# Kernel optimization log

Hardware: AMD Instinct MI355X
Metric: run time of the kernel (lower is better)

## Reference

```python
import jax, jax.numpy as jnp
import numpy as np

B, Lq, C, NH, NP, DFF = 8, 10000, 256, 8, 4, 1024
H_IMG, W_IMG = 100, 100
HD = C // NH


def _layer_norm(x, g, b, eps=1e-5):
    m = jnp.mean(x, -1, keepdims=True)
    v = jnp.mean((x - m) ** 2, -1, keepdims=True)
    return (x - m) / jnp.sqrt(v + eps) * g + b


def _bilinear_sample(value, loc, Hs, Ws):
    # value: [B, Lin, NH, HD]; loc: [B, Lq, NH, NP, 2] normalized to [0,1]
    vt = jnp.transpose(value, (0, 2, 1, 3))  # [B, NH, Lin, HD]
    # move to [B, NH, Lq, NP] layout once; grid_sample(align_corners=False) pixel coords
    x = jnp.transpose(loc[..., 0], (0, 2, 1, 3)) * Ws - 0.5
    y = jnp.transpose(loc[..., 1], (0, 2, 1, 3)) * Hs - 0.5
    x0 = jnp.floor(x); y0 = jnp.floor(y)
    lx = x - x0; ly = y - y0

    def corner(xi, yi, w):
        valid = (xi >= 0) & (xi < Ws) & (yi >= 0) & (yi < Hs)
        xc = jnp.clip(xi, 0, Ws - 1).astype(jnp.int32)
        yc = jnp.clip(yi, 0, Hs - 1).astype(jnp.int32)
        idx = (yc * Ws + xc).reshape(B, NH, Lq * NP, 1)
        v = jnp.take_along_axis(vt, idx, axis=2).reshape(B, NH, Lq, NP, HD)
        return v * (w * valid)[..., None]

    acc = corner(x0, y0, (1 - lx) * (1 - ly))
    acc = acc + corner(x0 + 1, y0, lx * (1 - ly))
    acc = acc + corner(x0, y0 + 1, (1 - lx) * ly)
    acc = acc + corner(x0 + 1, y0 + 1, lx * ly)
    return acc  # [B, NH, Lq, NP, HD]


def setup_inputs() -> dict:
    key = jax.random.key(0)
    ks = jax.random.split(key, 12)
    s = 0.02
    return {
        "query": jax.random.normal(ks[0], (B, Lq, C), jnp.float32),
        "src": jax.random.normal(ks[1], (B, H_IMG * W_IMG, C), jnp.float32),
        "reference_points": jax.random.uniform(ks[2], (B, Lq, 1, 2), jnp.float32),
        "spatial_shapes": jnp.array([[H_IMG, W_IMG]], dtype=jnp.int64),
        "level_start_index": jnp.array([0], dtype=jnp.int64),
        "W_off": jax.random.normal(ks[3], (C, NH * NP * 2), jnp.float32) * s,
        "b_off": jnp.zeros((NH * NP * 2,), jnp.float32),
        "W_aw": jax.random.normal(ks[4], (C, NH * NP), jnp.float32) * s,
        "b_aw": jnp.zeros((NH * NP,), jnp.float32),
        "W_val": jax.random.normal(ks[5], (C, C), jnp.float32) * s,
        "b_val": jnp.zeros((C,), jnp.float32),
        "W_out": jax.random.normal(ks[6], (C, C), jnp.float32) * s,
        "b_out": jnp.zeros((C,), jnp.float32),
        "g1": jnp.ones((C,), jnp.float32),
        "be1": jnp.zeros((C,), jnp.float32),
        "W1": jax.random.normal(ks[7], (C, DFF), jnp.float32) * s,
        "b1": jnp.zeros((DFF,), jnp.float32),
        "W2": jax.random.normal(ks[8], (DFF, C), jnp.float32) * s,
        "b2": jnp.zeros((C,), jnp.float32),
        "g2": jnp.ones((C,), jnp.float32),
        "be2": jnp.zeros((C,), jnp.float32),
    }


def reference(query, src, reference_points, spatial_shapes, level_start_index,
              W_off, b_off, W_aw, b_aw, W_val, b_val, W_out, b_out,
              g1, be1, W1, b1, W2, b2, g2, be2):
    Hs = spatial_shapes[0, 0]
    Ws = spatial_shapes[0, 1]
    # MSDeformAttn (n_levels = 1)
    value = (src @ W_val + b_val).reshape(B, -1, NH, HD)
    off = (query @ W_off + b_off).reshape(B, Lq, NH, NP, 2)
    aw = jax.nn.softmax((query @ W_aw + b_aw).reshape(B, Lq, NH, NP), axis=-1)
    normalizer = jnp.stack([Ws, Hs]).astype(query.dtype)  # (W, H)
    loc = reference_points[:, :, None] + off / normalizer  # [B,Lq,NH,NP,2]
    sampled = _bilinear_sample(value, loc, Hs, Ws)  # [B,NH,Lq,NP,HD]
    attn = jnp.einsum('bhqpd,bqhp->bqhd', sampled, aw).reshape(B, Lq, C)
    attn = attn @ W_out + b_out
    # residual + LN + FFN + LN
    q = _layer_norm(query + attn, g1, be1)
    ffn = jax.nn.relu(q @ W1 + b1) @ W2 + b2
    return _layer_norm(q + ffn, g2, be2)
```

## Files before the change

kernel.cpp:

```cpp
#include <hip/hip_runtime.h>
#include <hip/hip_bf16.h>

typedef __hip_bfloat16 bf16;
typedef unsigned short u16;
typedef short short8 __attribute__((ext_vector_type(8)));
typedef float f32x4 __attribute__((ext_vector_type(4)));

static constexpr int B_   = 8;
static constexpr int Lq_  = 10000;
static constexpr int C_   = 256;
static constexpr int NH_  = 8;
static constexpr int NP_  = 4;
static constexpr int HIMG = 100;
static constexpr int WIMG = 100;
static constexpr int LIN  = 10000;

__device__ __forceinline__ u16 f2bf(float x) {
    union { bf16 b; u16 u; } cv; cv.b = __float2bfloat16(x); return cv.u;
}
__device__ __forceinline__ float bf2f(u16 u) {
    return __uint_as_float((unsigned)u << 16);
}

__device__ __forceinline__ void gl_lds16(const void* g, void* l) {
    __builtin_amdgcn_global_load_lds(
        (const __attribute__((address_space(1))) void*)g,
        (__attribute__((address_space(3))) void*)l, 16, 0, 0);
}
__device__ __forceinline__ void drain_barrier() {
    asm volatile("s_waitcnt vmcnt(0) lgkmcnt(0)" ::: "memory");
    __builtin_amdgcn_s_barrier();
}


template <bool AF32, bool LN>
__global__ __launch_bounds__(512, 2) void gemm256(
    const void* __restrict__ Av, const u16* __restrict__ Bg,
    const float* __restrict__ bias, const float* __restrict__ resid,
    const float* __restrict__ gw, const float* __restrict__ bw,
    u16* __restrict__ Co, int K)
{
    __shared__ __align__(16) u16 At[2][128 * 64];
    __shared__ __align__(16) u16 Bt[2][256 * 64];
    __shared__ float red[2][128][4];

    const int tid  = threadIdx.x;
    const int lane = tid & 63;
    const int w    = tid >> 6;
    const int wm   = w >> 2, wn = w & 3;
    const int m0   = blockIdx.x * 128;

    f32x4 acc[4][4];
#pragma unroll
    for (int i = 0; i < 4; ++i)
#pragma unroll
        for (int j = 0; j < 4; ++j) acc[i][j] = f32x4{0.f, 0.f, 0.f, 0.f};

    auto stageA = [&](int t) {
        const int kt = t << 6;
        if constexpr (AF32) {
            const int row = tid >> 2;
            const int k0  = (tid & 3) << 4;
            const float* s = (const float*)Av + (size_t)(m0 + row) * K + kt + k0;
            float4 v0 = *(const float4*)(s + 0);
            float4 v1 = *(const float4*)(s + 4);
            float4 v2 = *(const float4*)(s + 8);
            float4 v3 = *(const float4*)(s + 12);
            union { short8 s8; u16 u[8]; } ga, gb;
            ga.u[0]=f2bf(v0.x); ga.u[1]=f2bf(v0.y); ga.u[2]=f2bf(v0.z); ga.u[3]=f2bf(v0.w);
            ga.u[4]=f2bf(v1.x); ga.u[5]=f2bf(v1.y); ga.u[6]=f2bf(v1.z); ga.u[7]=f2bf(v1.w);
            gb.u[0]=f2bf(v2.x); gb.u[1]=f2bf(v2.y); gb.u[2]=f2bf(v2.z); gb.u[3]=f2bf(v2.w);
            gb.u[4]=f2bf(v3.x); gb.u[5]=f2bf(v3.y); gb.u[6]=f2bf(v3.z); gb.u[7]=f2bf(v3.w);
            u16* d = &At[t & 1][row * 64];
            *(short8*)&d[(k0)     ^ ((row & 7) << 3)] = ga.s8;
            *(short8*)&d[(k0 + 8) ^ ((row & 7) << 3)] = gb.s8;
        } else {
#pragma unroll
            for (int i = 0; i < 2; ++i) {
                const int rb  = w * 16 + i * 8;
                const int row = rb + (lane >> 3);
                const int gs  = (lane & 7) ^ (row & 7);
                gl_lds16((const u16*)Av + (size_t)(m0 + row) * K + kt + gs * 8,
                         &At[t & 1][rb * 64]);
            }
        }
    };
    auto stageB = [&](int t) {
        const int kt = t << 6;
#pragma unroll
        for (int i = 0; i < 4; ++i) {
            const int rb  = w * 32 + i * 8;
            const int row = rb + (lane >> 3);
            gl_lds16(Bg + (size_t)row * K + kt + (lane & 7) * 8,
                     &Bt[t & 1][rb * 64]);
        }
    };
    auto compute = [&](int t) {
        const u16* a = At[t & 1];
        const u16* b = Bt[t & 1];
#pragma unroll
        for (int ks = 0; ks < 2; ++ks) {
            const int ko = ks * 32 + ((lane >> 4) << 3);
            short8 bfr[4];
#pragma unroll
            for (int n = 0; n < 4; ++n) {
                const int nr = wn * 64 + n * 16 + (lane & 15);
                bfr[n] = *(const short8*)&b[nr * 64 + (ko ^ ((nr & 7) << 3))];
            }
#pragma unroll
            for (int m = 0; m < 4; ++m) {
                const int ar = wm * 64 + m * 16 + (lane & 15);
                const short8 af = *(const short8*)&a[ar * 64 + (ko ^ ((ar & 7) << 3))];
#pragma unroll
                for (int n = 0; n < 4; ++n)
                    acc[m][n] = __builtin_amdgcn_mfma_f32_16x16x32_bf16(
                        af, bfr[n], acc[m][n], 0, 0, 0);
            }
        }
    };

    stageA(0); stageB(0);
    drain_barrier();
    const int nt = K >> 6;
    for (int t = 0; t < nt; ++t) {
        if (t + 1 < nt) { stageA(t + 1); stageB(t + 1); }
        compute(t);
        drain_barrier();
    }

    float bcol[4], gcol[4], becol[4];
#pragma unroll
    for (int n = 0; n < 4; ++n) {
        const int col = wn * 64 + n * 16 + (lane & 15);
        bcol[n] = bias[col];
        if (LN) { gcol[n] = gw[col]; becol[n] = bw[col]; }
    }

    if constexpr (!LN) {
#pragma unroll
        for (int m = 0; m < 4; ++m)
#pragma unroll
            for (int r = 0; r < 4; ++r) {
                const int lr = wm * 64 + m * 16 + (lane >> 4) * 4 + r;
#pragma unroll
                for (int n = 0; n < 4; ++n) {
                    const int col = wn * 64 + n * 16 + (lane & 15);
                    Co[(size_t)(m0 + lr) * 256 + col] = f2bf(acc[m][n][r] + bcol[n]);
                }
            }
    } else {
        float s[4][4], s2[4][4];
#pragma unroll
        for (int m = 0; m < 4; ++m)
#pragma unroll
            for (int r = 0; r < 4; ++r) {
                const int lr = wm * 64 + m * 16 + (lane >> 4) * 4 + r;
                float ps = 0.f, ps2 = 0.f;
#pragma unroll
                for (int n = 0; n < 4; ++n) {
                    const int col = wn * 64 + n * 16 + (lane & 15);
                    float v = acc[m][n][r] + bcol[n]
                            + resid[(size_t)(m0 + lr) * 256 + col];
                    acc[m][n][r] = v;
                    ps += v; ps2 += v * v;
                }
#pragma unroll
                for (int o = 1; o < 16; o <<= 1) {
                    ps  += __shfl_xor(ps,  o);
                    ps2 += __shfl_xor(ps2, o);
                }
                s[m][r] = ps; s2[m][r] = ps2;
            }
        if ((lane & 15) == 0) {
#pragma unroll
            for (int m = 0; m < 4; ++m)
#pragma unroll
                for (int r = 0; r < 4; ++r) {
                    const int lr = wm * 64 + m * 16 + (lane >> 4) * 4 + r;
                    red[0][lr][wn] = s[m][r];
                    red[1][lr][wn] = s2[m][r];
                }
        }
        __syncthreads();
        if (tid < 128) {
            const float ss  = red[0][tid][0] + red[0][tid][1] + red[0][tid][2] + red[0][tid][3];
            const float ss2 = red[1][tid][0] + red[1][tid][1] + red[1][tid][2] + red[1][tid][3];
            const float mean = ss * (1.f / 256.f);
            const float var  = fmaxf(ss2 * (1.f / 256.f) - mean * mean, 0.f);
            red[0][tid][0] = mean;
            red[1][tid][0] = rsqrtf(var + 1e-5f);
        }
        __syncthreads();
#pragma unroll
        for (int m = 0; m < 4; ++m)
#pragma unroll
            for (int r = 0; r < 4; ++r) {
                const int lr = wm * 64 + m * 16 + (lane >> 4) * 4 + r;
                const float mean = red[0][lr][0];
                const float rstd = red[1][lr][0];
#pragma unroll
                for (int n = 0; n < 4; ++n) {
                    const int col = wn * 64 + n * 16 + (lane & 15);
                    const float o = (acc[m][n][r] - mean) * rstd * gcol[n] + becol[n];
                    Co[(size_t)(m0 + lr) * 256 + (col ^ ((lr & 7) << 3))] = f2bf(o);
                }
            }
    }
}

__global__ __launch_bounds__(512, 2) void ffn_fused(
    const u16* __restrict__ q1b, const u16* __restrict__ W1s,
    const u16* __restrict__ W2s, const float* __restrict__ b1,
    const float* __restrict__ b2, const float* __restrict__ g2,
    const float* __restrict__ be2, float* __restrict__ out)
{
    __shared__ __align__(16) u16 As[128 * 256];
    __shared__ __align__(16) u16 Hs[128 * 128];
    __shared__ __align__(16) u16 B1t[2][128 * 32];
    __shared__ __align__(16) u16 B2t[2][256 * 32];
    __shared__ float red[2][128][4];

    const int tid  = threadIdx.x;
    const int lane = tid & 63;
    const int w    = tid >> 6;
    const int wm   = w >> 2, wn = w & 3;
    const int m0   = blockIdx.x * 128;

    f32x4 acc2[4][4];
#pragma unroll
    for (int i = 0; i < 4; ++i)
#pragma unroll
        for (int j = 0; j < 4; ++j) acc2[i][j] = f32x4{0.f, 0.f, 0.f, 0.f};

    auto stageB1 = [&](int c, int t) {
        const int rb  = w * 16;
        const int row = rb + (lane >> 2);
        gl_lds16(W1s + (size_t)(c * 128 + row) * 256 + t * 32 + (lane & 3) * 8,
                 &B1t[t & 1][rb * 32]);
    };
    auto stageB2 = [&](int c, int t) {
#pragma unroll
        for (int i = 0; i < 2; ++i) {
            const int rb  = i * 128 + w * 16;
            const int row = rb + (lane >> 2);
            gl_lds16(W2s + (size_t)row * 1024 + c * 128 + t * 32 + (lane & 3) * 8,
                     &B2t[t & 1][rb * 32]);
        }
    };

#pragma unroll
    for (int i = 0; i < 8; ++i) {
        const int rb = w * 16 + i * 2;
        gl_lds16(q1b + (size_t)(m0 + rb + (lane >> 5)) * 256 + (lane & 31) * 8,
                 &As[rb * 256]);
    }
    stageB1(0, 0);
    drain_barrier();

    for (int c = 0; c < 8; ++c) {
        f32x4 acc1[4][2];
#pragma unroll
        for (int i = 0; i < 4; ++i)
#pragma unroll
            for (int j = 0; j < 2; ++j) acc1[i][j] = f32x4{0.f, 0.f, 0.f, 0.f};

        for (int t = 0; t < 8; ++t) {
            if (t < 7) stageB1(c, t + 1);
            else       stageB2(c, 0);
            const u16* b = B1t[t & 1];
            const int ko = (lane >> 4) << 3;
            short8 bfr[2];
#pragma unroll
            for (int n = 0; n < 2; ++n) {
                const int nr = wn * 32 + n * 16 + (lane & 15);
                bfr[n] = *(const short8*)&b[nr * 32 + (ko ^ ((nr & 3) << 3))];
            }
#pragma unroll
            for (int m = 0; m < 4; ++m) {
                const int ar = wm * 64 + m * 16 + (lane & 15);
                const short8 af = *(const short8*)
                    &As[ar * 256 + ((t * 32 + ko) ^ ((ar & 7) << 3))];
#pragma unroll
                for (int n = 0; n < 2; ++n)
                    acc1[m][n] = __builtin_amdgcn_mfma_f32_16x16x32_bf16(
                        af, bfr[n], acc1[m][n], 0, 0, 0);
            }
            drain_barrier();
        }

#pragma unroll
        for (int n = 0; n < 2; ++n) {
            const int col = wn * 32 + n * 16 + (lane & 15);
            const float bb = b1[c * 128 + col];
#pragma unroll
            for (int m = 0; m < 4; ++m)
#pragma unroll
                for (int r = 0; r < 4; ++r) {
                    const int row = wm * 64 + m * 16 + (lane >> 4) * 4 + r;
                    const float hv = fmaxf(acc1[m][n][r] + bb, 0.f);
                    Hs[row * 128 + (col ^ ((row & 7) << 3))] = f2bf(hv);
                }
        }
        asm volatile("s_waitcnt lgkmcnt(0)" ::: "memory");
        __builtin_amdgcn_s_barrier();

        for (int t = 0; t < 4; ++t) {
            if (t < 3)      stageB2(c, t + 1);
            else if (c < 7) stageB1(c + 1, 0);
            const u16* b = B2t[t & 1];
            const int ko = (lane >> 4) << 3;
            short8 bfr[4];
#pragma unroll
            for (int n = 0; n < 4; ++n) {
                const int nr = wn * 64 + n * 16 + (lane & 15);
                bfr[n] = *(const short8*)&b[nr * 32 + (ko ^ ((nr & 3) << 3))];
            }
#pragma unroll
            for (int m = 0; m < 4; ++m) {
                const int hr = wm * 64 + m * 16 + (lane & 15);
                const short8 af = *(const short8*)
                    &Hs[hr * 128 + ((t * 32 + ko) ^ ((hr & 7) << 3))];
#pragma unroll
                for (int n = 0; n < 4; ++n)
                    acc2[m][n] = __builtin_amdgcn_mfma_f32_16x16x32_bf16(
                        af, bfr[n], acc2[m][n], 0, 0, 0);
            }
            drain_barrier();
        }
    }

    float bcol[4], gcol[4], becol[4];
#pragma unroll
    for (int n = 0; n < 4; ++n) {
        const int col = wn * 64 + n * 16 + (lane & 15);
        bcol[n] = b2[col]; gcol[n] = g2[col]; becol[n] = be2[col];
    }
    float s[4][4], s2[4][4];
#pragma unroll
    for (int m = 0; m < 4; ++m)
#pragma unroll
        for (int r = 0; r < 4; ++r) {
            const int lr = wm * 64 + m * 16 + (lane >> 4) * 4 + r;
            float ps = 0.f, ps2 = 0.f;
#pragma unroll
            for (int n = 0; n < 4; ++n) {
                const int col = wn * 64 + n * 16 + (lane & 15);
                const float q = bf2f(As[lr * 256 + (col ^ ((lr & 7) << 3))]);
                const float v = acc2[m][n][r] + bcol[n] + q;
                acc2[m][n][r] = v;
                ps += v; ps2 += v * v;
            }
#pragma unroll
            for (int o = 1; o < 16; o <<= 1) {
                ps  += __shfl_xor(ps,  o);
                ps2 += __shfl_xor(ps2, o);
            }
            s[m][r] = ps; s2[m][r] = ps2;
        }
    if ((lane & 15) == 0) {
#pragma unroll
        for (int m = 0; m < 4; ++m)
#pragma unroll
            for (int r = 0; r < 4; ++r) {
                const int lr = wm * 64 + m * 16 + (lane >> 4) * 4 + r;
                red[0][lr][wn] = s[m][r];
                red[1][lr][wn] = s2[m][r];
            }
    }
    __syncthreads();
    if (tid < 128) {
        const float ss  = red[0][tid][0] + red[0][tid][1] + red[0][tid][2] + red[0][tid][3];
        const float ss2 = red[1][tid][0] + red[1][tid][1] + red[1][tid][2] + red[1][tid][3];
        const float mean = ss * (1.f / 256.f);
        const float var  = fmaxf(ss2 * (1.f / 256.f) - mean * mean, 0.f);
        red[0][tid][0] = mean;
        red[1][tid][0] = rsqrtf(var + 1e-5f);
    }
    __syncthreads();
#pragma unroll
    for (int m = 0; m < 4; ++m)
#pragma unroll
        for (int r = 0; r < 4; ++r) {
            const int lr = wm * 64 + m * 16 + (lane >> 4) * 4 + r;
            const float mean = red[0][lr][0];
            const float rstd = red[1][lr][0];
#pragma unroll
            for (int n = 0; n < 4; ++n) {
                const int col = wn * 64 + n * 16 + (lane & 15);
                out[(size_t)(m0 + lr) * 256 + col] =
                    (acc2[m][n][r] - mean) * rstd * gcol[n] + becol[n];
            }
        }
}

__global__ __launch_bounds__(256) void gemm_oaw(
    const float* __restrict__ Av, const u16* __restrict__ Bt,
    const float* __restrict__ bias, float* __restrict__ C,
    int M, int K, int Nreal, int ldc)
{
    __shared__ __align__(16) u16 Asl[2][128 * 32];
    __shared__ __align__(16) u16 Bsl[2][128 * 32];

    const int tid  = threadIdx.x;
    const int lane = tid & 63;
    const int w    = tid >> 6;
    const int wr   = (w >> 1) * 64;
    const int wc   = (w & 1) * 64;
    const int m0   = blockIdx.y * 128;
    const int n0   = blockIdx.x * 128;

    const int srow = lane >> 2;
    const int scol = (lane & 3) << 3;
    const u16* bG = Bt + (size_t)(n0 + w * 32 + srow) * K + scol;
    const size_t rstep16 = (size_t)16 * K;

    const int ar  = lane >> 3;
    const int ac  = (lane & 7) << 2;
    const float* aGf = Av + (size_t)(m0 + w * 32 + ar) * K + ac;

    const int aRoff = (wr + (lane & 15)) * 32 + (lane >> 4) * 8;
    const int bRoff = (wc + (lane & 15)) * 32 + (lane >> 4) * 8;

    f32x4 acc[4][4];
#pragma unroll
    for (int i = 0; i < 4; ++i)
#pragma unroll
        for (int j = 0; j < 4; ++j) acc[i][j] = f32x4{0.f, 0.f, 0.f, 0.f};

    float4 a4[4];
    const int nt = K >> 5;

#pragma unroll
    for (int rep = 0; rep < 4; ++rep)
        a4[rep] = *(const float4*)(aGf + (size_t)(rep * 8) * K);
#pragma unroll
    for (int rep = 0; rep < 4; ++rep) {
        ushort4 v{f2bf(a4[rep].x), f2bf(a4[rep].y), f2bf(a4[rep].z), f2bf(a4[rep].w)};
        *(ushort4*)&Asl[0][(w * 32 + rep * 8 + ar) * 32 + ac] = v;
    }
    gl_lds16(bG, &Bsl[0][(w * 32) * 32]);
    gl_lds16(bG + rstep16, &Bsl[0][(w * 32 + 16) * 32]);
    drain_barrier();

    for (int t = 0; t < nt; ++t) {
        const int cur = t & 1, nxt = cur ^ 1;
        const int k0n = (t + 1) << 5;
        const bool has_next = (t + 1 < nt);
        if (has_next) {
#pragma unroll
            for (int rep = 0; rep < 4; ++rep)
                a4[rep] = *(const float4*)(aGf + k0n + (size_t)(rep * 8) * K);
            gl_lds16(bG + k0n, &Bsl[nxt][(w * 32) * 32]);
            gl_lds16(bG + k0n + rstep16, &Bsl[nxt][(w * 32 + 16) * 32]);
        }
        short8 af[4], bfr[4];
#pragma unroll
        for (int m = 0; m < 4; ++m) af[m]  = *(const short8*)&Asl[cur][aRoff + m * 16 * 32];
#pragma unroll
        for (int n = 0; n < 4; ++n) bfr[n] = *(const short8*)&Bsl[cur][bRoff + n * 16 * 32];
#pragma unroll
        for (int m = 0; m < 4; ++m)
#pragma unroll
            for (int n = 0; n < 4; ++n)
                acc[m][n] = __builtin_amdgcn_mfma_f32_16x16x32_bf16(
                    af[m], bfr[n], acc[m][n], 0, 0, 0);
        if (has_next) {
#pragma unroll
            for (int rep = 0; rep < 4; ++rep) {
                ushort4 v{f2bf(a4[rep].x), f2bf(a4[rep].y), f2bf(a4[rep].z), f2bf(a4[rep].w)};
                *(ushort4*)&Asl[nxt][(w * 32 + rep * 8 + ar) * 32 + ac] = v;
            }
        }
        drain_barrier();
    }

#pragma unroll
    for (int n = 0; n < 4; ++n) {
        const int gc = n0 + wc + n * 16 + (lane & 15);
        if (gc >= Nreal) continue;
        const float bv = bias[gc];
        const int gr0 = m0 + wr + (lane >> 4) * 4;
#pragma unroll
        for (int m = 0; m < 4; ++m)
#pragma unroll
            for (int r = 0; r < 4; ++r)
                C[(size_t)(gr0 + m * 16 + r) * ldc + gc] = acc[m][n][r] + bv;
    }
}

__global__ __launch_bounds__(256) void prep_all(
    const float* __restrict__ Wv, const float* __restrict__ Wo,
    const float* __restrict__ W1, const float* __restrict__ W2,
    const float* __restrict__ Woff, const float* __restrict__ Waw,
    const float* __restrict__ boff, const float* __restrict__ baw,
    u16* __restrict__ Wvs, u16* __restrict__ Wos,
    u16* __restrict__ W1s, u16* __restrict__ W2s,
    u16* __restrict__ Woa, float* __restrict__ boa)
{
    const int idx = blockIdx.x * 256 + threadIdx.x;
    if (idx < 65536) {
        const int n = idx >> 8, kd = idx & 255;
        Wvs[idx] = f2bf(Wv[(size_t)(kd ^ ((n & 7) << 3)) * 256 + n]);
    } else if (idx < 131072) {
        const int i = idx - 65536, n = i >> 8, kd = i & 255;
        Wos[i] = f2bf(Wo[(size_t)(kd ^ ((n & 7) << 3)) * 256 + n]);
    } else if (idx < 393216) {
        const int i = idx - 131072, n = i >> 8, kd = i & 255;
        W1s[i] = f2bf(W1[(size_t)(kd ^ ((n & 3) << 3)) * 1024 + n]);
    } else if (idx < 655360) {
        const int i = idx - 393216, n = i >> 10, kd = i & 1023;
        W2s[i] = f2bf(W2[(size_t)(kd ^ ((n & 3) << 3)) * 256 + n]);
    } else if (idx < 688128) {
        const int i = idx - 655360, n = i >> 8, k = i & 255;
        float v = 0.f;
        if (n < 64)      v = Woff[(size_t)k * 64 + n];
        else if (n < 96) v = Waw[(size_t)k * 32 + (n - 64)];
        Woa[i] = f2bf(v);
    } else if (idx < 688256) {
        const int i = idx - 688128;
        boa[i] = (i < 64) ? boff[i] : (i < 96 ? baw[i - 64] : 0.f);
    }
}

__global__ __launch_bounds__(256) void sample_attn(
    const u16* __restrict__ val, const float* __restrict__ oaw,
    const float* __restrict__ refp, u16* __restrict__ attn)
{
    const int t   = threadIdx.x;
    const int gid = blockIdx.x * 64 + (t >> 2);
    const int c0  = (t & 3) << 3;
    const int h   = gid & (NH_ - 1);
    const int bq  = gid >> 3;

    const float* row = oaw + (size_t)bq * 96;
    const float rx = refp[(size_t)bq * 2 + 0] * (float)WIMG;
    const float ry = refp[(size_t)bq * 2 + 1] * (float)HIMG;

    const float4 aw4 = *(const float4*)(row + 64 + h * 4);
    const float mx = fmaxf(fmaxf(aw4.x, aw4.y), fmaxf(aw4.z, aw4.w));
    const float e0 = __expf(aw4.x - mx), e1 = __expf(aw4.y - mx);
    const float e2 = __expf(aw4.z - mx), e3 = __expf(aw4.w - mx);
    const float inv = 1.f / (e0 + e1 + e2 + e3);
    const float w4[4] = {e0 * inv, e1 * inv, e2 * inv, e3 * inv};

    const int b = bq / Lq_;
    const u16* vb = val + (size_t)b * LIN * C_ + h * 32 + c0;

    float acc[8] = {};
#pragma unroll
    for (int p = 0; p < NP_; ++p) {
        const float2 off = *(const float2*)(row + (h * 4 + p) * 2);
        const float x = rx + off.x - 0.5f;
        const float y = ry + off.y - 0.5f;
        const float xf = floorf(x), yf = floorf(y);
        const float lx = x - xf, ly = y - yf;
        const int x0 = (int)xf, y0 = (int)yf;
        const float wp = w4[p];
        const float w00 = wp * (1.f - lx) * (1.f - ly);
        const float w10 = wp * lx * (1.f - ly);
        const float w01 = wp * (1.f - lx) * ly;
        const float w11 = wp * lx * ly;

#pragma unroll
        for (int c = 0; c < 4; ++c) {
            const int xi = x0 + (c & 1);
            const int yi = y0 + (c >> 1);
            const float wc = (c == 0) ? w00 : (c == 1) ? w10 : (c == 2) ? w01 : w11;
            const bool v = ((unsigned)xi < (unsigned)WIMG) & ((unsigned)yi < (unsigned)HIMG);
            const int idx = v ? (yi * WIMG + xi) : 0;
            const float w = v ? wc : 0.f;
            const short8 d = *(const short8*)(vb + (size_t)idx * C_);
#pragma unroll
            for (int j = 0; j < 8; ++j)
                acc[j] = fmaf(w, bf2f(((const u16*)&d)[j]), acc[j]);
        }
    }

    union { short8 s; u16 u[8]; } o;
#pragma unroll
    for (int j = 0; j < 8; ++j) o.u[j] = f2bf(acc[j]);
    *(short8*)(attn + (size_t)bq * C_ + h * 32 + c0) = o.s;
}

extern "C" void kernel_launch(void* const* d_in, const int* in_sizes, int n_in,
                              void* d_out, int out_size, void* d_ws, size_t ws_size,
                              hipStream_t stream)
{
    const float* query = (const float*)d_in[0];
    const float* src   = (const float*)d_in[1];
    const float* refp  = (const float*)d_in[2];
    const float* W_off = (const float*)d_in[5];
    const float* b_off = (const float*)d_in[6];
    const float* W_aw  = (const float*)d_in[7];
    const float* b_aw  = (const float*)d_in[8];
    const float* W_val = (const float*)d_in[9];
    const float* b_val = (const float*)d_in[10];
    const float* W_out = (const float*)d_in[11];
    const float* b_out = (const float*)d_in[12];
    const float* g1    = (const float*)d_in[13];
    const float* be1   = (const float*)d_in[14];
    const float* W1    = (const float*)d_in[15];
    const float* b1    = (const float*)d_in[16];
    const float* W2    = (const float*)d_in[17];
    const float* b2    = (const float*)d_in[18];
    const float* g2    = (const float*)d_in[19];
    const float* be2   = (const float*)d_in[20];
    float* out = (float*)d_out;

    char* ws = (char*)d_ws;
    const int R = B_ * Lq_;

    u16*  val  = (u16*)(ws + 0);
    float* oaw = (float*)(ws + 40960000);
    u16*  attn = (u16*)(ws + 71680000);
    u16*  q1b  = (u16*)(ws + 112640000);
    u16*  Wvs  = (u16*)(ws + 153600000);
    u16*  Wos  = (u16*)(ws + 153600000 + 131072);
    u16*  W1s  = (u16*)(ws + 153600000 + 262144);
    u16*  W2s  = (u16*)(ws + 153600000 + 786432);
    u16*  Woa  = (u16*)(ws + 153600000 + 1310720);
    float* boa = (float*)(ws + 153600000 + 1376256);

    prep_all<<<2689, 256, 0, stream>>>(W_val, W_out, W1, W2, W_off, W_aw,
                                       b_off, b_aw, Wvs, Wos, W1s, W2s,
                                       Woa, boa);

    gemm256<true, false><<<625, 512, 0, stream>>>(
        src, Wvs, b_val, nullptr, nullptr, nullptr, val, 256);

    gemm_oaw<<<dim3(1, 625), 256, 0, stream>>>(
        query, Woa, boa, oaw, R, 256, 96, 96);

    sample_attn<<<10000, 256, 0, stream>>>(val, oaw, refp, attn);

    gemm256<false, true><<<625, 512, 0, stream>>>(
        attn, Wos, b_out, query, g1, be1, q1b, 256);

    ffn_fused<<<625, 512, 0, stream>>>(q1b, W1s, W2s, b1, b2, g2, be2, out);
}
```

Measured before the change: 327.4 us.

## Triple-buffer W1 tiles in the fused FFN with partial vmcnt waits

Restructures the fused FFN kernel's weight-streaming pipeline. W1 tiles now use three LDS buffers and are prefetched several steps ahead. The full vmcnt(0) drain at every step is replaced by partial vmcnt waits, so global-to-LDS loads overlap the MFMA work across the GEMM1/GEMM2 boundary. The hidden tile drops its XOR swizzle for row padding, the LN reduction scratch is aliased onto it, and the occupancy hint in launch bounds is removed. On the last iteration the code prefetches W1 tiles for c+1=8, past the end of W1, with no guard, and the hand-counted vmcnt values must match exactly to stay correct.

```diff
diff --git a/kernel.cpp b/kernel.cpp
--- a/kernel.cpp
+++ b/kernel.cpp
@@ -31,6 +31,9 @@
     asm volatile("s_waitcnt vmcnt(0) lgkmcnt(0)" ::: "memory");
     __builtin_amdgcn_s_barrier();
 }
+#define VMW(N) asm volatile("s_waitcnt vmcnt(" #N ")" ::: "memory")
+#define LKW0() asm volatile("s_waitcnt lgkmcnt(0)" ::: "memory")
+#define BAR()  __builtin_amdgcn_s_barrier()
 
 
 template <bool AF32, bool LN>
@@ -208,17 +211,17 @@
     }
 }
 
-__global__ __launch_bounds__(512, 2) void ffn_fused(
+__global__ __launch_bounds__(512) void ffn_fused(
     const u16* __restrict__ q1b, const u16* __restrict__ W1s,
     const u16* __restrict__ W2s, const float* __restrict__ b1,
     const float* __restrict__ b2, const float* __restrict__ g2,
     const float* __restrict__ be2, float* __restrict__ out)
 {
     __shared__ __align__(16) u16 As[128 * 256];
-    __shared__ __align__(16) u16 Hs[128 * 128];
-    __shared__ __align__(16) u16 B1t[2][128 * 32];
+    __shared__ __align__(16) u16 Hs[128 * 136];
+    __shared__ __align__(16) u16 B1t[3][128 * 32];
     __shared__ __align__(16) u16 B2t[2][256 * 32];
-    __shared__ float red[2][128][4];
+    float (*red)[128][4] = (float (*)[128][4])Hs;
 
     const int tid  = threadIdx.x;
     const int lane = tid & 63;
@@ -232,19 +235,19 @@
 #pragma unroll
         for (int j = 0; j < 4; ++j) acc2[i][j] = f32x4{0.f, 0.f, 0.f, 0.f};
 
-    auto stageB1 = [&](int c, int t) {
+    auto issueB1 = [&](int c, int t, int buf) {
         const int rb  = w * 16;
         const int row = rb + (lane >> 2);
         gl_lds16(W1s + (size_t)(c * 128 + row) * 256 + t * 32 + (lane & 3) * 8,
-                 &B1t[t & 1][rb * 32]);
+                 &B1t[buf][rb * 32]);
     };
-    auto stageB2 = [&](int c, int t) {
+    auto issueB2 = [&](int c, int u, int buf) {
 #pragma unroll
         for (int i = 0; i < 2; ++i) {
             const int rb  = i * 128 + w * 16;
             const int row = rb + (lane >> 2);
-            gl_lds16(W2s + (size_t)row * 1024 + c * 128 + t * 32 + (lane & 3) * 8,
-                     &B2t[t & 1][rb * 32]);
+            gl_lds16(W2s + (size_t)row * 1024 + c * 128 + u * 32 + (lane & 3) * 8,
+                     &B2t[buf][rb * 32]);
         }
     };
 
@@ -254,8 +257,8 @@
         gl_lds16(q1b + (size_t)(m0 + rb + (lane >> 5)) * 256 + (lane & 31) * 8,
                  &As[rb * 256]);
     }
-    stageB1(0, 0);
-    drain_barrier();
+    issueB1(0, 0, 0); issueB1(0, 1, 1); issueB1(0, 2, 2);
+    VMW(2); BAR();
 
     for (int c = 0; c < 8; ++c) {
         f32x4 acc1[4][2];
@@ -264,16 +267,14 @@
 #pragma unroll
             for (int j = 0; j < 2; ++j) acc1[i][j] = f32x4{0.f, 0.f, 0.f, 0.f};
 
-        for (int t = 0; t < 8; ++t) {
-            if (t < 7) stageB1(c, t + 1);
-            else       stageB2(c, 0);
-            const u16* b = B1t[t & 1];
+        auto g1 = [&](int t, int buf) {
+            const u16* bb = B1t[buf];
             const int ko = (lane >> 4) << 3;
             short8 bfr[2];
 #pragma unroll
             for (int n = 0; n < 2; ++n) {
                 const int nr = wn * 32 + n * 16 + (lane & 15);
-                bfr[n] = *(const short8*)&b[nr * 32 + (ko ^ ((nr & 3) << 3))];
+                bfr[n] = *(const short8*)&bb[nr * 32 + (ko ^ ((nr & 3) << 3))];
             }
 #pragma unroll
             for (int m = 0; m < 4; ++m) {
@@ -285,8 +286,37 @@
                     acc1[m][n] = __builtin_amdgcn_mfma_f32_16x16x32_bf16(
                         af, bfr[n], acc1[m][n], 0, 0, 0);
             }
-            drain_barrier();
-        }
+        };
+        auto g2s = [&](int u, int buf) {
+            const u16* bb = B2t[buf];
+            const int ko = (lane >> 4) << 3;
+            short8 bfr[4];
+#pragma unroll
+            for (int n = 0; n < 4; ++n) {
+                const int nr = wn * 64 + n * 16 + (lane & 15);
+                bfr[n] = *(const short8*)&bb[nr * 32 + (ko ^ ((nr & 3) << 3))];
+            }
+#pragma unroll
+            for (int m = 0; m < 4; ++m) {
+                const int hr = wm * 64 + m * 16 + (lane & 15);
+                const short8 af = *(const short8*)&Hs[hr * 136 + u * 32 + ko];
+#pragma unroll
+                for (int n = 0; n < 4; ++n)
+                    acc2[m][n] = __builtin_amdgcn_mfma_f32_16x16x32_bf16(
+                        af, bfr[n], acc2[m][n], 0, 0, 0);
+            }
+        };
+
+        g1(0, 0);
+        if (c == 0) { VMW(1); } else { VMW(3); }
+        BAR();
+        issueB1(c, 3, 0); g1(1, 1); VMW(1); BAR();
+        issueB1(c, 4, 1); g1(2, 2); VMW(1); BAR();
+        issueB1(c, 5, 2); g1(3, 0); VMW(1); BAR();
+        issueB1(c, 6, 0); g1(4, 1); VMW(1); BAR();
+        issueB1(c, 7, 1); g1(5, 2); VMW(1); BAR();
+        issueB2(c, 0, 0); g1(6, 0); VMW(2); BAR();
+        issueB2(c, 1, 1); g1(7, 1); VMW(2); BAR();
 
 #pragma unroll
         for (int n = 0; n < 2; ++n) {
@@ -297,37 +327,18 @@
 #pragma unroll
                 for (int r = 0; r < 4; ++r) {
                     const int row = wm * 64 + m * 16 + (lane >> 4) * 4 + r;
-                    const float hv = fmaxf(acc1[m][n][r] + bb, 0.f);
-                    Hs[row * 128 + (col ^ ((row & 7) << 3))] = f2bf(hv);
+                    Hs[row * 136 + col] = f2bf(fmaxf(acc1[m][n][r] + bb, 0.f));
                 }
         }
-        asm volatile("s_waitcnt lgkmcnt(0)" ::: "memory");
-        __builtin_amdgcn_s_barrier();
-
-        for (int t = 0; t < 4; ++t) {
-            if (t < 3)      stageB2(c, t + 1);
-            else if (c < 7) stageB1(c + 1, 0);
-            const u16* b = B2t[t & 1];
-            const int ko = (lane >> 4) << 3;
-            short8 bfr[4];
-#pragma unroll
-            for (int n = 0; n < 4; ++n) {
-                const int nr = wn * 64 + n * 16 + (lane & 15);
-                bfr[n] = *(const short8*)&b[nr * 32 + (ko ^ ((nr & 3) << 3))];
-            }
-#pragma unroll
-            for (int m = 0; m < 4; ++m) {
-                const int hr = wm * 64 + m * 16 + (lane & 15);
-                const short8 af = *(const short8*)
-                    &Hs[hr * 128 + ((t * 32 + ko) ^ ((hr & 7) << 3))];
-#pragma unroll
-                for (int n = 0; n < 4; ++n)
-                    acc2[m][n] = __builtin_amdgcn_mfma_f32_16x16x32_bf16(
-                        af, bfr[n], acc2[m][n], 0, 0, 0);
-            }
-            drain_barrier();
-        }
-    }
+        LKW0(); BAR();
+
+        issueB1(c + 1, 0, 0);                    g2s(0, 0); VMW(1); BAR();
+        issueB2(c, 2, 0); issueB1(c + 1, 1, 1);  g2s(1, 1); VMW(1); BAR();
+        issueB2(c, 3, 1); issueB1(c + 1, 2, 2);  g2s(2, 0); VMW(1); BAR();
+        g2s(3, 1); VMW(6); BAR();
+    }
+    asm volatile("s_waitcnt vmcnt(0)" ::: "memory");
+    BAR();
 
     float bcol[4], gcol[4], becol[4];
 #pragma unroll
```

After: 310.9 us (median of 2 runs). 5.1% less time.

## Split fused FFN into two generic GEMM launches with HBM hidden buffer

Applied to the files above, without the earlier changes.

Replaces the fused FFN kernel, which kept the 1024-wide hidden activation in shared memory, with two launches of the generalized gemm256 template. The first computes relu(q1@W1+b1) into a bf16 hidden buffer in global memory, and the second computes h@W2 plus residual and LayerNorm. The GEMM template gains an N-block grid dimension, ReLU and bf16-residual epilogues, and per-64 swizzled weight layouts. This trades on-chip fusion for simpler, larger-tile GEMMs that should use the MFMA units better, at the cost of writing and reading a 164 MB hidden tensor through HBM and one extra launch.

```diff
diff --git a/kernel.cpp b/kernel.cpp
--- a/kernel.cpp
+++ b/kernel.cpp
@@ -32,13 +32,12 @@
     __builtin_amdgcn_s_barrier();
 }
 
-
-template <bool AF32, bool LN>
+template <int AMODE, int EPI>
 __global__ __launch_bounds__(512, 2) void gemm256(
     const void* __restrict__ Av, const u16* __restrict__ Bg,
-    const float* __restrict__ bias, const float* __restrict__ resid,
+    const float* __restrict__ bias, const void* __restrict__ resid,
     const float* __restrict__ gw, const float* __restrict__ bw,
-    u16* __restrict__ Co, int K)
+    void* __restrict__ Cv, int K, int ldc)
 {
     __shared__ __align__(16) u16 At[2][128 * 64];
     __shared__ __align__(16) u16 Bt[2][256 * 64];
@@ -49,6 +48,8 @@
     const int w    = tid >> 6;
     const int wm   = w >> 2, wn = w & 3;
     const int m0   = blockIdx.x * 128;
+    const int n0   = blockIdx.y * 256;
+    const u16* BgB = Bg + (size_t)n0 * K;
 
     f32x4 acc[4][4];
 #pragma unroll
@@ -58,7 +59,7 @@
 
     auto stageA = [&](int t) {
         const int kt = t << 6;
-        if constexpr (AF32) {
+        if constexpr (AMODE == 0) {
             const int row = tid >> 2;
             const int k0  = (tid & 3) << 4;
             const float* s = (const float*)Av + (size_t)(m0 + row) * K + kt + k0;
@@ -74,7 +75,7 @@
             u16* d = &At[t & 1][row * 64];
             *(short8*)&d[(k0)     ^ ((row & 7) << 3)] = ga.s8;
             *(short8*)&d[(k0 + 8) ^ ((row & 7) << 3)] = gb.s8;
-        } else {
+        } else if constexpr (AMODE == 1) {
 #pragma unroll
             for (int i = 0; i < 2; ++i) {
                 const int rb  = w * 16 + i * 8;
@@ -83,6 +84,14 @@
                 gl_lds16((const u16*)Av + (size_t)(m0 + row) * K + kt + gs * 8,
                          &At[t & 1][rb * 64]);
             }
+        } else {
+#pragma unroll
+            for (int i = 0; i < 2; ++i) {
+                const int rb  = w * 16 + i * 8;
+                const int row = rb + (lane >> 3);
+                gl_lds16((const u16*)Av + (size_t)(m0 + row) * K + kt + (lane & 7) * 8,
+                         &At[t & 1][rb * 64]);
+            }
         }
     };
     auto stageB = [&](int t) {
@@ -91,7 +100,7 @@
         for (int i = 0; i < 4; ++i) {
             const int rb  = w * 32 + i * 8;
             const int row = rb + (lane >> 3);
-            gl_lds16(Bg + (size_t)row * K + kt + (lane & 7) * 8,
+            gl_lds16(BgB + (size_t)row * K + kt + (lane & 7) * 8,
                      &Bt[t & 1][rb * 64]);
         }
     };
@@ -132,11 +141,12 @@
 #pragma unroll
     for (int n = 0; n < 4; ++n) {
         const int col = wn * 64 + n * 16 + (lane & 15);
-        bcol[n] = bias[col];
-        if (LN) { gcol[n] = gw[col]; becol[n] = bw[col]; }
-    }
-
-    if constexpr (!LN) {
+        bcol[n] = bias[n0 + col];
+        if (EPI >= 2) { gcol[n] = gw[col]; becol[n] = bw[col]; }
+    }
+
+    if constexpr (EPI <= 1) {
+        u16* Co = (u16*)Cv;
 #pragma unroll
         for (int m = 0; m < 4; ++m)
 #pragma unroll
@@ -145,7 +155,9 @@
 #pragma unroll
                 for (int n = 0; n < 4; ++n) {
                     const int col = wn * 64 + n * 16 + (lane & 15);
-                    Co[(size_t)(m0 + lr) * 256 + col] = f2bf(acc[m][n][r] + bcol[n]);
+                    float v = acc[m][n][r] + bcol[n];
+                    if (EPI == 1) v = fmaxf(v, 0.f);
+                    Co[(size_t)(m0 + lr) * ldc + n0 + col] = f2bf(v);
                 }
             }
     } else {
@@ -159,8 +171,13 @@
 #pragma unroll
                 for (int n = 0; n < 4; ++n) {
                     const int col = wn * 64 + n * 16 + (lane & 15);
-                    float v = acc[m][n][r] + bcol[n]
-                            + resid[(size_t)(m0 + lr) * 256 + col];
+                    float rv;
+                    if constexpr (EPI == 2)
+                        rv = ((const float*)resid)[(size_t)(m0 + lr) * 256 + col];
+                    else
+                        rv = bf2f(((const u16*)resid)[(size_t)(m0 + lr) * 256
+                                                      + (col ^ ((lr & 7) << 3))]);
+                    float v = acc[m][n][r] + bcol[n] + rv;
                     acc[m][n][r] = v;
                     ps += v; ps2 += v * v;
                 }
@@ -202,195 +219,13 @@
                 for (int n = 0; n < 4; ++n) {
                     const int col = wn * 64 + n * 16 + (lane & 15);
                     const float o = (acc[m][n][r] - mean) * rstd * gcol[n] + becol[n];
-                    Co[(size_t)(m0 + lr) * 256 + (col ^ ((lr & 7) << 3))] = f2bf(o);
+                    if constexpr (EPI == 2)
+                        ((u16*)Cv)[(size_t)(m0 + lr) * 256 + (col ^ ((lr & 7) << 3))] = f2bf(o);
+                    else
+                        ((float*)Cv)[(size_t)(m0 + lr) * 256 + col] = o;
                 }
             }
     }
-}
-
-__global__ __launch_bounds__(512, 2) void ffn_fused(
-    const u16* __restrict__ q1b, const u16* __restrict__ W1s,
-    const u16* __restrict__ W2s, const float* __restrict__ b1,
-    const float* __restrict__ b2, const float* __restrict__ g2,
-    const float* __restrict__ be2, float* __restrict__ out)
-{
-    __shared__ __align__(16) u16 As[128 * 256];
-    __shared__ __align__(16) u16 Hs[128 * 128];
-    __shared__ __align__(16) u16 B1t[2][128 * 32];
-    __shared__ __align__(16) u16 B2t[2][256 * 32];
-    __shared__ float red[2][128][4];
-
-    const int tid  = threadIdx.x;
-    const int lane = tid & 63;
-    const int w    = tid >> 6;
-    const int wm   = w >> 2, wn = w & 3;
-    const int m0   = blockIdx.x * 128;
-
-    f32x4 acc2[4][4];
-#pragma unroll
-    for (int i = 0; i < 4; ++i)
-#pragma unroll
-        for (int j = 0; j < 4; ++j) acc2[i][j] = f32x4{0.f, 0.f, 0.f, 0.f};
-
-    auto stageB1 = [&](int c, int t) {
-        const int rb  = w * 16;
-        const int row = rb + (lane >> 2);
-        gl_lds16(W1s + (size_t)(c * 128 + row) * 256 + t * 32 + (lane & 3) * 8,
-                 &B1t[t & 1][rb * 32]);
-    };
-    auto stageB2 = [&](int c, int t) {
-#pragma unroll
-        for (int i = 0; i < 2; ++i) {
-            const int rb  = i * 128 + w * 16;
-            const int row = rb + (lane >> 2);
-            gl_lds16(W2s + (size_t)row * 1024 + c * 128 + t * 32 + (lane & 3) * 8,
-                     &B2t[t & 1][rb * 32]);
-        }
-    };
-
-#pragma unroll
-    for (int i = 0; i < 8; ++i) {
-        const int rb = w * 16 + i * 2;
-        gl_lds16(q1b + (size_t)(m0 + rb + (lane >> 5)) * 256 + (lane & 31) * 8,
-                 &As[rb * 256]);
-    }
-    stageB1(0, 0);
-    drain_barrier();
-
-    for (int c = 0; c < 8; ++c) {
-        f32x4 acc1[4][2];
-#pragma unroll
-        for (int i = 0; i < 4; ++i)
-#pragma unroll
-            for (int j = 0; j < 2; ++j) acc1[i][j] = f32x4{0.f, 0.f, 0.f, 0.f};
-
-        for (int t = 0; t < 8; ++t) {
-            if (t < 7) stageB1(c, t + 1);
-            else       stageB2(c, 0);
-            const u16* b = B1t[t & 1];
-            const int ko = (lane >> 4) << 3;
-            short8 bfr[2];
-#pragma unroll
-            for (int n = 0; n < 2; ++n) {
-                const int nr = wn * 32 + n * 16 + (lane & 15);
-                bfr[n] = *(const short8*)&b[nr * 32 + (ko ^ ((nr & 3) << 3))];
-            }
-#pragma unroll
-            for (int m = 0; m < 4; ++m) {
-                const int ar = wm * 64 + m * 16 + (lane & 15);
-                const short8 af = *(const short8*)
-                    &As[ar * 256 + ((t * 32 + ko) ^ ((ar & 7) << 3))];
-#pragma unroll
-                for (int n = 0; n < 2; ++n)
-                    acc1[m][n] = __builtin_amdgcn_mfma_f32_16x16x32_bf16(
-                        af, bfr[n], acc1[m][n], 0, 0, 0);
-            }
-            drain_barrier();
-        }
-
-#pragma unroll
-        for (int n = 0; n < 2; ++n) {
-            const int col = wn * 32 + n * 16 + (lane & 15);
-            const float bb = b1[c * 128 + col];
-#pragma unroll
-            for (int m = 0; m < 4; ++m)
-#pragma unroll
-                for (int r = 0; r < 4; ++r) {
-                    const int row = wm * 64 + m * 16 + (lane >> 4) * 4 + r;
-                    const float hv = fmaxf(acc1[m][n][r] + bb, 0.f);
-                    Hs[row * 128 + (col ^ ((row & 7) << 3))] = f2bf(hv);
-                }
-        }
-        asm volatile("s_waitcnt lgkmcnt(0)" ::: "memory");
-        __builtin_amdgcn_s_barrier();
-
-        for (int t = 0; t < 4; ++t) {
-            if (t < 3)      stageB2(c, t + 1);
-            else if (c < 7) stageB1(c + 1, 0);
-            const u16* b = B2t[t & 1];
-            const int ko = (lane >> 4) << 3;
-            short8 bfr[4];
-#pragma unroll
-            for (int n = 0; n < 4; ++n) {
-                const int nr = wn * 64 + n * 16 + (lane & 15);
-                bfr[n] = *(const short8*)&b[nr * 32 + (ko ^ ((nr & 3) << 3))];
-            }
-#pragma unroll
-            for (int m = 0; m < 4; ++m) {
-                const int hr = wm * 64 + m * 16 + (lane & 15);
-                const short8 af = *(const short8*)
-                    &Hs[hr * 128 + ((t * 32 + ko) ^ ((hr & 7) << 3))];
-#pragma unroll
-                for (int n = 0; n < 4; ++n)
-                    acc2[m][n] = __builtin_amdgcn_mfma_f32_16x16x32_bf16(
-                        af, bfr[n], acc2[m][n], 0, 0, 0);
-            }
-            drain_barrier();
-        }
-    }
-
-    float bcol[4], gcol[4], becol[4];
-#pragma unroll
-    for (int n = 0; n < 4; ++n) {
-        const int col = wn * 64 + n * 16 + (lane & 15);
-        bcol[n] = b2[col]; gcol[n] = g2[col]; becol[n] = be2[col];
-    }
-    float s[4][4], s2[4][4];
-#pragma unroll
-    for (int m = 0; m < 4; ++m)
-#pragma unroll
-        for (int r = 0; r < 4; ++r) {
-            const int lr = wm * 64 + m * 16 + (lane >> 4) * 4 + r;
-            float ps = 0.f, ps2 = 0.f;
-#pragma unroll
-            for (int n = 0; n < 4; ++n) {
-                const int col = wn * 64 + n * 16 + (lane & 15);
-                const float q = bf2f(As[lr * 256 + (col ^ ((lr & 7) << 3))]);
-                const float v = acc2[m][n][r] + bcol[n] + q;
-                acc2[m][n][r] = v;
-                ps += v; ps2 += v * v;
-            }
-#pragma unroll
-            for (int o = 1; o < 16; o <<= 1) {
-                ps  += __shfl_xor(ps,  o);
-                ps2 += __shfl_xor(ps2, o);
-            }
-            s[m][r] = ps; s2[m][r] = ps2;
-        }
-    if ((lane & 15) == 0) {
-#pragma unroll
-        for (int m = 0; m < 4; ++m)
-#pragma unroll
-            for (int r = 0; r < 4; ++r) {
-                const int lr = wm * 64 + m * 16 + (lane >> 4) * 4 + r;
-                red[0][lr][wn] = s[m][r];
-                red[1][lr][wn] = s2[m][r];
-            }
-    }
-    __syncthreads();
-    if (tid < 128) {
-        const float ss  = red[0][tid][0] + red[0][tid][1] + red[0][tid][2] + red[0][tid][3];
-        const float ss2 = red[1][tid][0] + red[1][tid][1] + red[1][tid][2] + red[1][tid][3];
-        const float mean = ss * (1.f / 256.f);
-        const float var  = fmaxf(ss2 * (1.f / 256.f) - mean * mean, 0.f);
-        red[0][tid][0] = mean;
-        red[1][tid][0] = rsqrtf(var + 1e-5f);
-    }
-    __syncthreads();
-#pragma unroll
-    for (int m = 0; m < 4; ++m)
-#pragma unroll
-        for (int r = 0; r < 4; ++r) {
-            const int lr = wm * 64 + m * 16 + (lane >> 4) * 4 + r;
-            const float mean = red[0][lr][0];
-            const float rstd = red[1][lr][0];
-#pragma unroll
-            for (int n = 0; n < 4; ++n) {
-                const int col = wn * 64 + n * 16 + (lane & 15);
-                out[(size_t)(m0 + lr) * 256 + col] =
-                    (acc2[m][n][r] - mean) * rstd * gcol[n] + becol[n];
-            }
-        }
 }
 
 __global__ __launch_bounds__(256) void gemm_oaw(
@@ -494,22 +329,26 @@
     const float* __restrict__ Woff, const float* __restrict__ Waw,
     const float* __restrict__ boff, const float* __restrict__ baw,
     u16* __restrict__ Wvs, u16* __restrict__ Wos,
-    u16* __restrict__ W1s, u16* __restrict__ W2s,
+    u16* __restrict__ W1g, u16* __restrict__ W2g,
     u16* __restrict__ Woa, float* __restrict__ boa)
 {
     const int idx = blockIdx.x * 256 + threadIdx.x;
     if (idx < 65536) {
         const int n = idx >> 8, kd = idx & 255;
-        Wvs[idx] = f2bf(Wv[(size_t)(kd ^ ((n & 7) << 3)) * 256 + n]);
+        const int k = (kd & ~63) | ((kd & 63) ^ ((n & 7) << 3));
+        Wvs[idx] = f2bf(Wv[(size_t)k * 256 + n]);
     } else if (idx < 131072) {
         const int i = idx - 65536, n = i >> 8, kd = i & 255;
-        Wos[i] = f2bf(Wo[(size_t)(kd ^ ((n & 7) << 3)) * 256 + n]);
+        const int k = (kd & ~63) | ((kd & 63) ^ ((n & 7) << 3));
+        Wos[i] = f2bf(Wo[(size_t)k * 256 + n]);
     } else if (idx < 393216) {
         const int i = idx - 131072, n = i >> 8, kd = i & 255;
-        W1s[i] = f2bf(W1[(size_t)(kd ^ ((n & 3) << 3)) * 1024 + n]);
+        const int k = (kd & ~63) | ((kd & 63) ^ ((n & 7) << 3));
+        W1g[i] = f2bf(W1[(size_t)k * 1024 + n]);
     } else if (idx < 655360) {
         const int i = idx - 393216, n = i >> 10, kd = i & 1023;
-        W2s[i] = f2bf(W2[(size_t)(kd ^ ((n & 3) << 3)) * 256 + n]);
+        const int k = (kd & ~63) | ((kd & 63) ^ ((n & 7) << 3));
+        W2g[i] = f2bf(W2[(size_t)k * 256 + n]);
     } else if (idx < 688128) {
         const int i = idx - 655360, n = i >> 8, k = i & 255;
         float v = 0.f;
@@ -608,33 +447,37 @@
     float* out = (float*)d_out;
 
     char* ws = (char*)d_ws;
-    const int R = B_ * Lq_;
 
     u16*  val  = (u16*)(ws + 0);
     float* oaw = (float*)(ws + 40960000);
     u16*  attn = (u16*)(ws + 71680000);
     u16*  q1b  = (u16*)(ws + 112640000);
-    u16*  Wvs  = (u16*)(ws + 153600000);
-    u16*  Wos  = (u16*)(ws + 153600000 + 131072);
-    u16*  W1s  = (u16*)(ws + 153600000 + 262144);
-    u16*  W2s  = (u16*)(ws + 153600000 + 786432);
-    u16*  Woa  = (u16*)(ws + 153600000 + 1310720);
-    float* boa = (float*)(ws + 153600000 + 1376256);
+    u16*  h    = (u16*)(ws + 153600000);
+    u16*  Wvs  = (u16*)(ws + 317440000);
+    u16*  Wos  = (u16*)(ws + 317440000 + 131072);
+    u16*  W1g  = (u16*)(ws + 317440000 + 262144);
+    u16*  W2g  = (u16*)(ws + 317440000 + 786432);
+    u16*  Woa  = (u16*)(ws + 317440000 + 1310720);
+    float* boa = (float*)(ws + 317440000 + 1376256);
 
     prep_all<<<2689, 256, 0, stream>>>(W_val, W_out, W1, W2, W_off, W_aw,
-                                       b_off, b_aw, Wvs, Wos, W1s, W2s,
+                                       b_off, b_aw, Wvs, Wos, W1g, W2g,
                                        Woa, boa);
 
-    gemm256<true, false><<<625, 512, 0, stream>>>(
-        src, Wvs, b_val, nullptr, nullptr, nullptr, val, 256);
+    gemm256<0, 0><<<dim3(625, 1), 512, 0, stream>>>(
+        src, Wvs, b_val, nullptr, nullptr, nullptr, val, 256, 256);
 
     gemm_oaw<<<dim3(1, 625), 256, 0, stream>>>(
-        query, Woa, boa, oaw, R, 256, 96, 96);
+        query, Woa, boa, oaw, B_ * Lq_, 256, 96, 96);
 
     sample_attn<<<10000, 256, 0, stream>>>(val, oaw, refp, attn);
 
-    gemm256<false, true><<<625, 512, 0, stream>>>(
-        attn, Wos, b_out, query, g1, be1, q1b, 256);
-
-    ffn_fused<<<625, 512, 0, stream>>>(q1b, W1s, W2s, b1, b2, g2, be2, out);
-}
+    gemm256<1, 2><<<dim3(625, 1), 512, 0, stream>>>(
+        attn, Wos, b_out, query, g1, be1, q1b, 256, 256);
+
+    gemm256<2, 1><<<dim3(625, 4), 512, 0, stream>>>(
+        q1b, W1g, b1, nullptr, nullptr, nullptr, h, 256, 1024);
+
+    gemm256<1, 3><<<dim3(625, 1), 512, 0, stream>>>(
+        h, W2g, b2, q1b, g2, be2, out, 1024, 256);
+}
```

Measured after the change: 360.4 us. 10.1% more time.
